# Performance work log

Measured on AMD Instinct MI355X. Metric: run time of the kernel, lower is better.

Reference implementation:

```python
import jax, jax.numpy as jnp
import numpy as np

B, H, S, D = 1, 16, 2048, 64


def setup_inputs() -> dict:
    key = jax.random.key(0)
    kq, kk, kv, km = jax.random.split(key, 4)
    q = jax.random.normal(kq, (B, H, S, D), dtype=jnp.float32)
    k = jax.random.normal(kk, (B, H, S, D), dtype=jnp.float32)
    v = jax.random.normal(kv, (B, H, S, D), dtype=jnp.float32)
    omask = jax.random.uniform(km, (B, H, S, S), dtype=jnp.float32)
    return {"q": q, "k": k, "v": v, "omask": omask}


def reference(q, k, v, omask):
    # mask = omask / sqrt(rowsum(omask)), nan -> 0
    row_sum = jnp.sum(omask, axis=-1, keepdims=True)  # [B,H,S,1]
    decay_mask = jnp.nan_to_num(omask / jnp.sqrt(row_sum), nan=0.0)
    # retention = (q k^T) * mask  -> [B,H,S,S]
    retention = jnp.einsum("bhsd,bhtd->bhst", q, k) * decay_mask
    # normalize by |rowsum(retention)| clamped to >= 1 (detached in original)
    scale = jnp.clip(jnp.abs(jnp.sum(retention, axis=-1, keepdims=True)), 1.0, None)
    retention = retention / scale
    # output = retention @ v -> [B,H,S,D]
    return jnp.einsum("bhst,bhtd->bhsd", retention, v)
```

## Files before the change

### kernel.cpp

```cpp
#include <hip/hip_runtime.h>

#define H 16
#define S 2048
#define D 64
#define BM 64
#define BN 64
#define NT (S / BN)

typedef __attribute__((ext_vector_type(8))) short bf16x8;
typedef __attribute__((ext_vector_type(4))) short short4v;
typedef __attribute__((ext_vector_type(4))) float fx4;
typedef __attribute__((ext_vector_type(16))) float f32x16;

static __device__ __forceinline__ short f2bf(float x) {
    unsigned u = __float_as_uint(x);
    u += 0x7fffu + ((u >> 16) & 1u);
    return (short)(u >> 16);
}
static __device__ __forceinline__ float bf2f(short s) {
    return __uint_as_float(((unsigned)(unsigned short)s) << 16);
}
static __device__ __forceinline__ void gl_lds16(const void* g, void* l) {
    __builtin_amdgcn_global_load_lds(
        (const __attribute__((address_space(1))) unsigned int*)g,
        (__attribute__((address_space(3))) unsigned int*)l, 16, 0, 0);
}

__global__ __launch_bounds__(256)
void ParallelRetention_prep_kernel(
    const float* __restrict__ k, const float* __restrict__ v,
    short* __restrict__ khi, short* __restrict__ klo, short* __restrict__ vt)
{
    __shared__ short lv[64 * 72];
    const int tid = threadIdx.x;
    const int h  = blockIdx.x & 15;
    const int sb = blockIdx.x >> 4;
    const int s0 = sb * 64;
    const int t_base = (tid >> 4) << 2;
    const int d4     = (tid & 15) << 2;
    const size_t hoff = (size_t)h * S * D;

    {
        const float* kb = k + hoff + (size_t)(s0 + t_base) * D + d4;
#pragma unroll
        for (int r = 0; r < 4; ++r) {
            fx4 kr = *(const fx4*)(kb + (size_t)r * D);
            short4v h4, l4;
#pragma unroll
            for (int j = 0; j < 4; ++j) {
                short hi = f2bf(kr[j]);
                h4[j] = hi;
                l4[j] = f2bf(kr[j] - bf2f(hi));
            }
            *(short4v*)(&khi[hoff + (size_t)(s0 + t_base + r) * D + d4]) = h4;
            *(short4v*)(&klo[hoff + (size_t)(s0 + t_base + r) * D + d4]) = l4;
        }
    }
    {
        const float* vb = v + hoff + (size_t)(s0 + t_base) * D + d4;
        fx4 vr[4];
#pragma unroll
        for (int r = 0; r < 4; ++r) vr[r] = *(const fx4*)(vb + (size_t)r * D);
#pragma unroll
        for (int j = 0; j < 4; ++j) {
            short4v p;
#pragma unroll
            for (int r = 0; r < 4; ++r) p[r] = f2bf(vr[r][j]);
            *(short4v*)(&lv[(d4 + j) * 72 + t_base]) = p;
        }
    }
    __syncthreads();
    {
        const int d = tid >> 2;
        const int c = tid & 3;
        bf16x8 a = *(const bf16x8*)(&lv[d * 72 + c * 16]);
        bf16x8 b = *(const bf16x8*)(&lv[d * 72 + c * 16 + 8]);
        short* o = vt + (size_t)h * D * S + (size_t)d * S + s0 + c * 16;
        *(bf16x8*)(o)     = a;
        *(bf16x8*)(o + 8) = b;
    }
}

__global__ __launch_bounds__(256, 2)
void ParallelRetention_origin_25374666785438_kernel(
    const float* __restrict__ q, const float* __restrict__ om,
    const short* __restrict__ khi, const short* __restrict__ klo,
    const short* __restrict__ vt, float* __restrict__ out)
{
    __shared__ short ldsKh[2][64 * 64];
    __shared__ short ldsKl[2][64 * 64];
    __shared__ short ldsVT[2][64 * 64];
    __shared__ short ldsP[4][32 * 64];

    const int tid  = threadIdx.x;
    const int wave = tid >> 6;
    const int lane = tid & 63;
    const int rg   = wave >> 1;
    const int khd  = wave & 1;
    const int ql   = lane & 31;
    const int hi   = lane >> 5;
    const int col16 = lane & 15;
    const int quad  = lane >> 4;

    const int h  = blockIdx.x & 15;
    const int qb = blockIdx.x >> 4;
    const int row0 = qb * BM;

    const size_t headQK = (size_t)h * S * D;
    const size_t headM  = (size_t)h * S * S;

    bf16x8 qh[4], qlo[4];
    {
        const float* qp = q + headQK + (size_t)(row0 + rg * 32 + ql) * D + hi * 8;
#pragma unroll
        for (int c = 0; c < 4; ++c) {
            fx4 a = *(const fx4*)(qp + c * 16);
            fx4 b = *(const fx4*)(qp + c * 16 + 4);
            float f[8] = {a[0],a[1],a[2],a[3],b[0],b[1],b[2],b[3]};
#pragma unroll
            for (int j = 0; j < 8; ++j) {
                short s = f2bf(f[j]);
                qh[c][j]  = s;
                qlo[c][j] = f2bf(f[j] - bf2f(s));
            }
        }
    }

    fx4 U[2][4];
#pragma unroll
    for (int qs = 0; qs < 2; ++qs)
#pragma unroll
        for (int nt = 0; nt < 4; ++nt) { U[qs][nt][0]=0.f; U[qs][nt][1]=0.f; U[qs][nt][2]=0.f; U[qs][nt][3]=0.f; }
    float rs_acc = 0.f, T_acc = 0.f;

    const int krow = khd * 32 + ql;
    int rdK[4];
#pragma unroll
    for (int c = 0; c < 4; ++c)
        rdK[c] = krow * 64 + ((((c << 1) + hi) ^ (ql & 7)) << 3);
    int vtOff[4];
#pragma unroll
    for (int nt = 0; nt < 4; ++nt)
        vtOff[nt] = (nt * 16 + col16) * 64 + (((khd * 4 + quad) ^ (col16 & 7)) << 3);
    int prOff[2];
#pragma unroll
    for (int qs = 0; qs < 2; ++qs)
        prOff[qs] = (qs * 16 + col16) * 64 + ((quad ^ (col16 & 7)) << 3);

    const int rowl = lane >> 3;
    const int swz8 = ((lane & 7) ^ rowl) * 8;
    const int kSrcOff = rowl * 64 + swz8;
    const int vSrcOff = rowl * 2048 + swz8;

    const short* khiH = khi + headQK;
    const short* kloH = klo + headQK;
    const short* vtH  = vt + (size_t)h * D * S;
    const float* omp0 = om + headM + (size_t)(row0 + rg * 32 + ql) * S + khd * 32 + hi * 4;

    auto stage = [&](int t0, short* dKh, short* dKl, short* dVT) {
        const short* ks = khiH + (size_t)t0 * 64 + kSrcOff;
        const short* ls = kloH + (size_t)t0 * 64 + kSrcOff;
        const short* vs = vtH + t0 + vSrcOff;
#pragma unroll
        for (int c = 0; c < 6; ++c) {
            int id = wave * 6 + c;
            int j  = id & 7;
            int tile = id >> 3;
            if (tile == 0)      gl_lds16(ks + j * 512, dKh + j * 512);
            else if (tile == 1) gl_lds16(ls + j * 512, dKl + j * 512);
            else                gl_lds16(vs + (size_t)j * 8 * 2048, dVT + j * 512);
        }
    };
    auto load_om = [&](int t0, fx4 (&o)[4]) {
#pragma unroll
        for (int g = 0; g < 4; ++g)
            o[g] = *(const fx4*)(omp0 + t0 + g * 8);
    };
    auto compute = [&](const short* Kh, const short* Kl, const short* VT,
                       const fx4 (&omc)[4]) {
        bf16x8 kh[4], kl[4];
#pragma unroll
        for (int c = 0; c < 4; ++c) {
            kh[c] = *(const bf16x8*)(&Kh[rdK[c]]);
            kl[c] = *(const bf16x8*)(&Kl[rdK[c]]);
        }
        f32x16 za, zb;
#pragma unroll
        for (int i = 0; i < 16; ++i) { za[i] = 0.f; zb[i] = 0.f; }
#pragma unroll
        for (int c = 0; c < 4; ++c) za = __builtin_amdgcn_mfma_f32_32x32x16_bf16(kh[c], qh[c],  za, 0, 0, 0);
#pragma unroll
        for (int c = 0; c < 4; ++c) zb = __builtin_amdgcn_mfma_f32_32x32x16_bf16(kl[c], qh[c],  zb, 0, 0, 0);
#pragma unroll
        for (int c = 0; c < 4; ++c) zb = __builtin_amdgcn_mfma_f32_32x32x16_bf16(kh[c], qlo[c], zb, 0, 0, 0);
        short* Pw = &ldsP[wave][0];
#pragma unroll
        for (int g = 0; g < 4; ++g) {
            short4v p4;
#pragma unroll
            for (int r = 0; r < 4; ++r) {
                float m = omc[g][r];
                float p = (za[g * 4 + r] + zb[g * 4 + r]) * m;
                rs_acc += m;
                T_acc  += p;
                p4[r] = f2bf(p);
            }
            *(short4v*)(&Pw[ql * 64 + ((g ^ (ql & 7)) << 3) + hi * 4]) = p4;
        }
        bf16x8 vb[4];
#pragma unroll
        for (int nt = 0; nt < 4; ++nt) vb[nt] = *(const bf16x8*)(&VT[vtOff[nt]]);
#pragma unroll
        for (int qs = 0; qs < 2; ++qs) {
            bf16x8 pa = *(const bf16x8*)(&Pw[prOff[qs]]);
#pragma unroll
            for (int nt = 0; nt < 4; ++nt)
                U[qs][nt] = __builtin_amdgcn_mfma_f32_16x16x32_bf16(pa, vb[nt], U[qs][nt], 0, 0, 0);
        }
    };

    fx4 omA[4], omB[4];
    stage(0, &ldsKh[0][0], &ldsKl[0][0], &ldsVT[0][0]);
    load_om(0, omA);

    for (int t = 0; t < NT; t += 2) {
        __syncthreads();
        if (t + 1 < NT) {
            stage((t + 1) * BN, &ldsKh[1][0], &ldsKl[1][0], &ldsVT[1][0]);
            load_om((t + 1) * BN, omB);
        }
        compute(&ldsKh[0][0], &ldsKl[0][0], &ldsVT[0][0], omA);
        __syncthreads();
        if (t + 2 < NT) {
            stage((t + 2) * BN, &ldsKh[0][0], &ldsKl[0][0], &ldsVT[0][0]);
            load_om((t + 2) * BN, omA);
        }
        compute(&ldsKh[1][0], &ldsKl[1][0], &ldsVT[1][0], omB);
    }

    rs_acc += __shfl_xor(rs_acc, 32, 64);
    T_acc  += __shfl_xor(T_acc, 32, 64);
    __syncthreads();
    float* scrU = (float*)&ldsKh[0][0];
    float* scrS = (float*)&ldsKl[0][0];
    if (khd == 1) {
#pragma unroll
        for (int qs = 0; qs < 2; ++qs)
#pragma unroll
            for (int nt = 0; nt < 4; ++nt)
#pragma unroll
                for (int r = 0; r < 4; ++r)
                    scrU[rg * 2048 + (qs * 16 + quad * 4 + r) * 64 + nt * 16 + col16] = U[qs][nt][r];
        if (lane < 32) {
            scrS[rg * 32 + ql] = rs_acc;
            scrS[64 + rg * 32 + ql] = T_acc;
        }
    }
    __syncthreads();
    if (khd == 0) {
        float rs = rs_acc + scrS[rg * 32 + ql];
        float Tt = T_acc + scrS[64 + rg * 32 + ql];
        float inv = rs > 0.f ? rsqrtf(rs) : 0.f;
        float sc = fabsf(Tt * inv);
        sc = sc < 1.f ? 1.f : sc;
        float fac = inv / sc;
        float* op = out + headQK + (size_t)(row0 + rg * 32) * D;
#pragma unroll
        for (int qs = 0; qs < 2; ++qs)
#pragma unroll
            for (int r = 0; r < 4; ++r) {
                float f = __shfl(fac, qs * 16 + quad * 4 + r, 64);
#pragma unroll
                for (int nt = 0; nt < 4; ++nt) {
                    float u = U[qs][nt][r] +
                        scrU[rg * 2048 + (qs * 16 + quad * 4 + r) * 64 + nt * 16 + col16];
                    op[(size_t)(qs * 16 + quad * 4 + r) * D + nt * 16 + col16] = u * f;
                }
            }
    }
}

extern "C" void kernel_launch(void* const* d_in, const int* in_sizes, int n_in,
                              void* d_out, int out_size, void* d_ws, size_t ws_size,
                              hipStream_t stream) {
    const float* q  = (const float*)d_in[0];
    const float* k  = (const float*)d_in[1];
    const float* v  = (const float*)d_in[2];
    const float* om = (const float*)d_in[3];
    float* out = (float*)d_out;
    (void)in_sizes; (void)n_in; (void)out_size; (void)ws_size;

    short* khi = (short*)d_ws;
    short* klo = khi + (size_t)H * S * D;
    short* vt  = klo + (size_t)H * S * D;

    hipLaunchKernelGGL(ParallelRetention_prep_kernel,
                       dim3(H * (S / 64)), dim3(256), 0, stream, k, v, khi, klo, vt);
    hipLaunchKernelGGL(ParallelRetention_origin_25374666785438_kernel,
                       dim3(H * (S / BM)), dim3(256), 0, stream, q, om, khi, klo, vt, out);
}
```

Baseline: 398.6 us.

## Keep P in registers via permlane32 swap and 32x32 MFMA for PV

Replaces the LDS round trip for the probability tile (write P to shared memory, read back in MFMA A-layout) with an in-register transpose using v_permlane32_swap and packed bf16 pairs. The PV product is reformulated as transposed 32x32x16 MFMAs (V^T times P^T), so each lane's accumulator holds its own query row and the epilogue can write contiguous float4 rows without shuffles. This removes LDS write/read traffic and the associated waits per tile, and frees the ldsP buffer. The risk is correctness of the lane/layout mapping and some added register pressure from the larger accumulators.

```diff
diff --git a/kernel.cpp b/kernel.cpp
--- a/kernel.cpp
+++ b/kernel.cpp
@@ -19,6 +19,9 @@
 }
 static __device__ __forceinline__ float bf2f(short s) {
     return __uint_as_float(((unsigned)(unsigned short)s) << 16);
+}
+static __device__ __forceinline__ unsigned pk2(float a, float b) {
+    return (unsigned)(unsigned short)f2bf(a) | ((unsigned)(unsigned short)f2bf(b) << 16);
 }
 static __device__ __forceinline__ void gl_lds16(const void* g, void* l) {
     __builtin_amdgcn_global_load_lds(
@@ -90,7 +93,6 @@
     __shared__ short ldsKh[2][64 * 64];
     __shared__ short ldsKl[2][64 * 64];
     __shared__ short ldsVT[2][64 * 64];
-    __shared__ short ldsP[4][32 * 64];
 
     const int tid  = threadIdx.x;
     const int wave = tid >> 6;
@@ -99,8 +101,6 @@
     const int khd  = wave & 1;
     const int ql   = lane & 31;
     const int hi   = lane >> 5;
-    const int col16 = lane & 15;
-    const int quad  = lane >> 4;
 
     const int h  = blockIdx.x & 15;
     const int qb = blockIdx.x >> 4;
@@ -126,11 +126,11 @@
         }
     }
 
-    fx4 U[2][4];
-#pragma unroll
-    for (int qs = 0; qs < 2; ++qs)
-#pragma unroll
-        for (int nt = 0; nt < 4; ++nt) { U[qs][nt][0]=0.f; U[qs][nt][1]=0.f; U[qs][nt][2]=0.f; U[qs][nt][3]=0.f; }
+    f32x16 Ut[2];
+#pragma unroll
+    for (int b = 0; b < 2; ++b)
+#pragma unroll
+        for (int i = 0; i < 16; ++i) Ut[b][i] = 0.f;
     float rs_acc = 0.f, T_acc = 0.f;
 
     const int krow = khd * 32 + ql;
@@ -138,14 +138,13 @@
 #pragma unroll
     for (int c = 0; c < 4; ++c)
         rdK[c] = krow * 64 + ((((c << 1) + hi) ^ (ql & 7)) << 3);
-    int vtOff[4];
-#pragma unroll
-    for (int nt = 0; nt < 4; ++nt)
-        vtOff[nt] = (nt * 16 + col16) * 64 + (((khd * 4 + quad) ^ (col16 & 7)) << 3);
-    int prOff[2];
-#pragma unroll
-    for (int qs = 0; qs < 2; ++qs)
-        prOff[qs] = (qs * 16 + col16) * 64 + ((quad ^ (col16 & 7)) << 3);
+    int vtOff[2][2];
+#pragma unroll
+    for (int dblk = 0; dblk < 2; ++dblk)
+#pragma unroll
+        for (int kt = 0; kt < 2; ++kt)
+            vtOff[dblk][kt] = (dblk * 32 + ql) * 64 +
+                (((khd * 4 + kt * 2 + hi) ^ (ql & 7)) << 3);
 
     const int rowl = lane >> 3;
     const int swz8 = ((lane & 7) ^ rowl) * 8;
@@ -193,29 +192,33 @@
         for (int c = 0; c < 4; ++c) zb = __builtin_amdgcn_mfma_f32_32x32x16_bf16(kl[c], qh[c],  zb, 0, 0, 0);
 #pragma unroll
         for (int c = 0; c < 4; ++c) zb = __builtin_amdgcn_mfma_f32_32x32x16_bf16(kh[c], qlo[c], zb, 0, 0, 0);
-        short* Pw = &ldsP[wave][0];
+        unsigned W[4][2];
 #pragma unroll
         for (int g = 0; g < 4; ++g) {
-            short4v p4;
+            float p[4];
 #pragma unroll
             for (int r = 0; r < 4; ++r) {
                 float m = omc[g][r];
-                float p = (za[g * 4 + r] + zb[g * 4 + r]) * m;
+                p[r] = (za[g * 4 + r] + zb[g * 4 + r]) * m;
                 rs_acc += m;
-                T_acc  += p;
-                p4[r] = f2bf(p);
-            }
-            *(short4v*)(&Pw[ql * 64 + ((g ^ (ql & 7)) << 3) + hi * 4]) = p4;
-        }
-        bf16x8 vb[4];
-#pragma unroll
-        for (int nt = 0; nt < 4; ++nt) vb[nt] = *(const bf16x8*)(&VT[vtOff[nt]]);
-#pragma unroll
-        for (int qs = 0; qs < 2; ++qs) {
-            bf16x8 pa = *(const bf16x8*)(&Pw[prOff[qs]]);
-#pragma unroll
-            for (int nt = 0; nt < 4; ++nt)
-                U[qs][nt] = __builtin_amdgcn_mfma_f32_16x16x32_bf16(pa, vb[nt], U[qs][nt], 0, 0, 0);
+                T_acc  += p[r];
+            }
+            W[g][0] = pk2(p[0], p[1]);
+            W[g][1] = pk2(p[2], p[3]);
+        }
+        union PB { unsigned w[4]; bf16x8 v; };
+#pragma unroll
+        for (int kt = 0; kt < 2; ++kt) {
+            unsigned x0 = W[2 * kt][0], y0 = W[2 * kt + 1][0];
+            unsigned x1 = W[2 * kt][1], y1 = W[2 * kt + 1][1];
+            asm volatile("v_permlane32_swap_b32 %0, %1" : "+v"(x0), "+v"(y0));
+            asm volatile("v_permlane32_swap_b32 %0, %1" : "+v"(x1), "+v"(y1));
+            PB pb; pb.w[0] = x0; pb.w[1] = x1; pb.w[2] = y0; pb.w[3] = y1;
+#pragma unroll
+            for (int dblk = 0; dblk < 2; ++dblk) {
+                bf16x8 va = *(const bf16x8*)(&VT[vtOff[dblk][kt]]);
+                Ut[dblk] = __builtin_amdgcn_mfma_f32_32x32x16_bf16(va, pb.v, Ut[dblk], 0, 0, 0);
+            }
         }
     };
 
@@ -245,13 +248,15 @@
     float* scrS = (float*)&ldsKl[0][0];
     if (khd == 1) {
 #pragma unroll
-        for (int qs = 0; qs < 2; ++qs)
-#pragma unroll
-            for (int nt = 0; nt < 4; ++nt)
-#pragma unroll
-                for (int r = 0; r < 4; ++r)
-                    scrU[rg * 2048 + (qs * 16 + quad * 4 + r) * 64 + nt * 16 + col16] = U[qs][nt][r];
-        if (lane < 32) {
+        for (int dblk = 0; dblk < 2; ++dblk)
+#pragma unroll
+            for (int g = 0; g < 4; ++g) {
+                fx4 u;
+#pragma unroll
+                for (int r = 0; r < 4; ++r) u[r] = Ut[dblk][g * 4 + r];
+                *(fx4*)(&scrU[rg * 2048 + ql * 64 + dblk * 32 + g * 8 + hi * 4]) = u;
+            }
+        if (hi == 0) {
             scrS[rg * 32 + ql] = rs_acc;
             scrS[64 + rg * 32 + ql] = T_acc;
         }
@@ -264,18 +269,17 @@
         float sc = fabsf(Tt * inv);
         sc = sc < 1.f ? 1.f : sc;
         float fac = inv / sc;
-        float* op = out + headQK + (size_t)(row0 + rg * 32) * D;
-#pragma unroll
-        for (int qs = 0; qs < 2; ++qs)
-#pragma unroll
-            for (int r = 0; r < 4; ++r) {
-                float f = __shfl(fac, qs * 16 + quad * 4 + r, 64);
-#pragma unroll
-                for (int nt = 0; nt < 4; ++nt) {
-                    float u = U[qs][nt][r] +
-                        scrU[rg * 2048 + (qs * 16 + quad * 4 + r) * 64 + nt * 16 + col16];
-                    op[(size_t)(qs * 16 + quad * 4 + r) * D + nt * 16 + col16] = u * f;
-                }
+        float* op = out + headQK + (size_t)(row0 + rg * 32 + ql) * D;
+#pragma unroll
+        for (int dblk = 0; dblk < 2; ++dblk)
+#pragma unroll
+            for (int g = 0; g < 4; ++g) {
+                const int d0 = dblk * 32 + g * 8 + hi * 4;
+                fx4 u;
+#pragma unroll
+                for (int r = 0; r < 4; ++r)
+                    u[r] = (Ut[dblk][g * 4 + r] + scrU[rg * 2048 + ql * 64 + d0 + r]) * fac;
+                *(fx4*)(&op[d0]) = u;
             }
     }
 }
```

Result: no change. 399.6 us (+0.3%).
